# Kernel tuning notes

Hardware: AMD Instinct MI355X
Metric: run time of the kernel (lower is better)

The kernel has to match this reference:

```python
import itertools
import jax, jax.numpy as jnp
import numpy as np

NUM_MOLS = 1024
N_ATOMS = 32  # atoms per molecule (< 50 per module's precomputed edge_indices)
Z_DIM = 64
HIDDEN = 256
NUM_ATOM_TYPES = 10
NUM_BOND_TYPES = 5  # hparams['num_bond_types'] + 1
BN_EPS = 1e-5


def _build_edge_index():
    base = np.array(list(itertools.combinations(range(N_ATOMS), 2)), dtype=np.int64)  # [496, 2]
    offsets = (N_ATOMS * np.arange(NUM_MOLS, dtype=np.int64))[:, None, None]
    return jnp.asarray((base[None] + offsets).reshape(-1, 2))  # [E, 2]


def setup_inputs() -> dict:
    key = jax.random.key(0)
    ks = jax.random.split(key, 4)
    total_atoms = NUM_MOLS * N_ATOMS
    return {
        "z": jax.random.normal(ks[0], (total_atoms, Z_DIM), dtype=jnp.float32),
        "W1": jax.random.normal(ks[1], (Z_DIM, HIDDEN), dtype=jnp.float32) * 0.05,
        "b1": jnp.zeros((HIDDEN,), jnp.float32),
        "bn_gamma": jnp.ones((HIDDEN,), jnp.float32),
        "bn_beta": jnp.zeros((HIDDEN,), jnp.float32),
        "W2": jax.random.normal(ks[2], (HIDDEN, NUM_ATOM_TYPES), dtype=jnp.float32) * 0.05,
        "b2": jnp.zeros((NUM_ATOM_TYPES,), jnp.float32),
        "bond_matrix": jax.random.normal(ks[3], (NUM_BOND_TYPES, Z_DIM, Z_DIM), dtype=jnp.float32),
        "edge_index": _build_edge_index(),
    }


def reference(z, W1, b1, bn_gamma, bn_beta, W2, b2, bond_matrix, edge_index):
    # atom classifier: Linear -> BatchNorm1d (training-mode batch stats) -> GELU -> Linear
    h = z @ W1 + b1  # [A, H]
    mean = jnp.mean(h, axis=0)
    var = jnp.mean((h - mean) ** 2, axis=0)  # biased variance, as torch BN
    h = (h - mean) * jax.lax.rsqrt(var + BN_EPS) * bn_gamma + bn_beta
    h = jax.nn.gelu(h, approximate=False)
    atom_types = h @ W2 + b2  # [A, num_atom_types]

    # symmetric bond matrices, per-edge bilinear quadratic form, softmax over bond types
    W = 0.5 * (bond_matrix + jnp.swapaxes(bond_matrix, 1, 2))  # [T, d, d]
    z1 = z[edge_index[:, 0]]  # [E, d]
    z2 = z[edge_index[:, 1]]  # [E, d]
    logits = jnp.einsum('ed,tdc,ec->et', z1, W, z2)  # [E, T]
    edge_types = jax.nn.softmax(logits, axis=1)
    return atom_types, edge_types
```

## Files before the change

kernel.cpp:

```cpp
#include <hip/hip_runtime.h>
#include <hip/hip_bf16.h>
#include <math.h>

#define NM 1024
#define NA 32
#define ZD 64
#define HD 256
#define AT 10
#define BT 5
#define NROWS (NM*NA)
#define EPM 496
#define ATOM_OUT (NROWS*AT)


__global__ __launch_bounds__(256) void k1_moments(const float* __restrict__ z,
                                                  float* __restrict__ Msum,
                                                  float* __restrict__ sumz) {
    __shared__ __align__(16) float zs[128][64];
    __shared__ float sred[4][64];
    const int tid = threadIdx.x;
    const int d0 = (tid >> 4) << 2;
    const int e0 = (tid & 15) << 2;
    const int d = tid & 63, rq = tid >> 6;
    float acc[4][4] = {};
    float colsum = 0.f;
    for (int chunk = 0; chunk < 2; ++chunk) {
        const int rowbase = (blockIdx.x * 2 + chunk) * 128;
        __syncthreads();
        const float4* zg4 = (const float4*)(z + rowbase * 64);
        float4* zs4 = (float4*)zs;
        #pragma unroll
        for (int k = 0; k < 8; ++k) zs4[tid + (k << 8)] = zg4[tid + (k << 8)];
        __syncthreads();
        for (int r = 0; r < 128; ++r) {
            float4 a4 = *(const float4*)&zs[r][d0];
            float4 b4 = *(const float4*)&zs[r][e0];
            float a[4] = {a4.x, a4.y, a4.z, a4.w};
            float b[4] = {b4.x, b4.y, b4.z, b4.w};
            #pragma unroll
            for (int i = 0; i < 4; ++i)
                #pragma unroll
                for (int jj = 0; jj < 4; ++jj) acc[i][jj] += a[i] * b[jj];
        }
        for (int r = rq * 32; r < rq * 32 + 32; ++r) colsum += zs[r][d];
    }
    #pragma unroll
    for (int i = 0; i < 4; ++i)
        #pragma unroll
        for (int jj = 0; jj < 4; ++jj)
            atomicAdd(&Msum[(d0 + i) * 64 + (e0 + jj)], acc[i][jj]);
    sred[rq][d] = colsum;
    __syncthreads();
    if (tid < 64)
        atomicAdd(&sumz[tid], sred[0][tid] + sred[1][tid] + sred[2][tid] + sred[3][tid]);
}

__global__ __launch_bounds__(256) void k2w(const float* __restrict__ Msum,
                                           const float* __restrict__ sumz,
                                           const float* __restrict__ W1,
                                           const float* __restrict__ gamma,
                                           const float* __restrict__ beta,
                                           const float* __restrict__ bond,
                                           float* __restrict__ avec,
                                           float* __restrict__ cvec,
                                           float* __restrict__ Wsym) {
    const int tid = threadIdx.x;
    if (blockIdx.x >= 64) {
        int idx = ((int)blockIdx.x - 64) * 256 + tid;
        int t = idx >> 12, rem = idx & 4095, dd = rem >> 6, c = rem & 63;
        Wsym[idx] = 0.5f * (bond[(t << 12) + (dd << 6) + c] +
                            bond[(t << 12) + (c << 6) + dd]);
        return;
    }
    const int wv = tid >> 6, d = tid & 63;
    const int j = blockIdx.x * 4 + wv;
    const float wdj = W1[d * HD + j];
    float v = 0.f;
    for (int e = 0; e < 64; ++e) v += Msum[d * 64 + e] * W1[e * HD + j];
    float q = v * wdj;
    float s = sumz[d] * wdj;
    #pragma unroll
    for (int off = 32; off >= 1; off >>= 1) {
        q += __shfl_down(q, off);
        s += __shfl_down(s, off);
    }
    if (d == 0) {
        const float invN = 1.f / (float)NROWS;
        float mean = s * invN;
        float var = q * invN - mean * mean;
        float a = gamma[j] * rsqrtf(var + 1e-5f);
        avec[j] = a;
        cvec[j] = beta[j] - mean * a;
    }
}

__global__ __launch_bounds__(256) void k3_mlp(const float* __restrict__ z,
                                              const float* __restrict__ W1,
                                              const float* __restrict__ W2,
                                              const float* __restrict__ b2,
                                              const float* __restrict__ avec,
                                              const float* __restrict__ cvec,
                                              float* __restrict__ out_atom) {
    __shared__ __align__(16) float zsT[64][36];
    __shared__ __align__(16) float w1s[16][256];
    __shared__ float w2s[256][11];
    __shared__ float as[256], cs[256];
    const int tid = threadIdx.x;
    const int rowbase = blockIdx.x * 32;
    {
        const float* zp = z + (size_t)(rowbase + (tid >> 3)) * 64 + (tid & 7) * 8;
        float4 v0 = *(const float4*)zp;
        float4 v1 = *(const float4*)(zp + 4);
        const int r = tid >> 3, dbase = (tid & 7) * 8;
        zsT[dbase + 0][r] = v0.x; zsT[dbase + 1][r] = v0.y;
        zsT[dbase + 2][r] = v0.z; zsT[dbase + 3][r] = v0.w;
        zsT[dbase + 4][r] = v1.x; zsT[dbase + 5][r] = v1.y;
        zsT[dbase + 6][r] = v1.z; zsT[dbase + 7][r] = v1.w;
    }
    for (int k = tid; k < HD * AT; k += 256) w2s[k / 10][k % 10] = W2[k];
    as[tid] = avec[tid]; cs[tid] = cvec[tid];

    const int rg = tid >> 4, cg = tid & 15;
    const int r0 = rg << 1;
    float acc[2][4][4] = {};
    for (int ch = 0; ch < 4; ++ch) {
        __syncthreads();
        #pragma unroll
        for (int k = 0; k < 16; ++k) {
            int idx = tid + (k << 8);
            ((float*)w1s)[idx] = W1[(ch << 12) + idx];
        }
        __syncthreads();
        #pragma unroll
        for (int dl = 0; dl < 16; ++dl) {
            float zr0 = zsT[(ch << 4) + dl][r0];
            float zr1 = zsT[(ch << 4) + dl][r0 + 1];
            #pragma unroll
            for (int cb = 0; cb < 4; ++cb) {
                float4 wv = *(const float4*)&w1s[dl][(cb << 6) + (cg << 2)];
                float wr[4] = {wv.x, wv.y, wv.z, wv.w};
                #pragma unroll
                for (int u = 0; u < 4; ++u) {
                    acc[0][cb][u] += zr0 * wr[u];
                    acc[1][cb][u] += zr1 * wr[u];
                }
            }
        }
    }
    float p[2][10] = {};
    #pragma unroll
    for (int cb = 0; cb < 4; ++cb)
        #pragma unroll
        for (int u = 0; u < 4; ++u) {
            const int c = (cb << 6) + (cg << 2) + u;
            const float a = as[c], cc = cs[c];
            #pragma unroll
            for (int ri = 0; ri < 2; ++ri) {
                float h = acc[ri][cb][u] * a + cc;
                h = 0.5f * h * (1.0f + erff(h * 0.70710678118654752f));
                #pragma unroll
                for (int o = 0; o < 10; ++o) p[ri][o] += h * w2s[c][o];
            }
        }
    #pragma unroll
    for (int m = 1; m <= 8; m <<= 1)
        #pragma unroll
        for (int ri = 0; ri < 2; ++ri)
            #pragma unroll
            for (int o = 0; o < 10; ++o) p[ri][o] += __shfl_xor(p[ri][o], m);
    if (cg == 0) {
        #pragma unroll
        for (int ri = 0; ri < 2; ++ri)
            for (int o = 0; o < 10; ++o)
                out_atom[(size_t)(rowbase + r0 + ri) * AT + o] = p[ri][o] + b2[o];
    }
}

__global__ __launch_bounds__(512) void k4_edges(const float* __restrict__ z,
                                                const float* __restrict__ Wsym,
                                                float* __restrict__ out_edge) {
    __shared__ float zs[2][32][66];
    __shared__ float uT[2][5][32][18];
    const int tid = threadIdx.x;
    const int mol0 = blockIdx.x * 2;
    {
        const float2* zg2 = (const float2*)(z + (size_t)mol0 * 2048);
        #pragma unroll
        for (int k = 0; k < 4; ++k) {
            int e = tid + (k << 9);
            int ml = e >> 10, r = (e >> 5) & 31, c2 = e & 31;
            float2 v = zg2[e];
            zs[ml][r][c2 * 2] = v.x;
            zs[ml][r][c2 * 2 + 1] = v.y;
        }
    }
    const int wv = __builtin_amdgcn_readfirstlane(tid >> 6);
    const int lane = tid & 63;
    const int molA = lane >> 5, jA = lane & 31;
    const int mlB = tid >> 8;
    const int jg = tid & 31;
    const int i0 = ((tid >> 5) & 7) << 2;
    float accE[5][4] = {};
    __syncthreads();

    for (int qd = 0; qd < 4; ++qd) {
        float accA[5][2] = {};
        const int dpos = (qd << 4) + (wv << 1);
        for (int cb = 0; cb < 4; ++cb) {
            float zr[16];
            #pragma unroll
            for (int m = 0; m < 8; ++m) {
                float2 v = *(const float2*)&zs[molA][jA][(cb << 4) + (m << 1)];
                zr[m * 2] = v.x; zr[m * 2 + 1] = v.y;
            }
            #pragma unroll
            for (int t = 0; t < 5; ++t) {
                const float* wbase = Wsym + (size_t)(t << 12) + (size_t)(cb << 10) + dpos;
                #pragma unroll
                for (int cc = 0; cc < 16; ++cc) {
                    float w0 = wbase[cc * 64];
                    float w1 = wbase[cc * 64 + 1];
                    accA[t][0] += w0 * zr[cc];
                    accA[t][1] += w1 * zr[cc];
                }
            }
        }
        __syncthreads();
        #pragma unroll
        for (int t = 0; t < 5; ++t) {
            float2 w; w.x = accA[t][0]; w.y = accA[t][1];
            *(float2*)&uT[molA][t][jA][wv << 1] = w;
        }
        __syncthreads();
        #pragma unroll
        for (int cq = 0; cq < 4; ++cq) {
            const int gd = (qd << 4) + (cq << 2);
            float zc[4][4];
            #pragma unroll
            for (int ri = 0; ri < 4; ++ri) {
                float2 a = *(const float2*)&zs[mlB][i0 + ri][gd];
                float2 b = *(const float2*)&zs[mlB][i0 + ri][gd + 2];
                zc[ri][0] = a.x; zc[ri][1] = a.y; zc[ri][2] = b.x; zc[ri][3] = b.y;
            }
            #pragma unroll
            for (int t = 0; t < 5; ++t) {
                float2 ua = *(const float2*)&uT[mlB][t][jg][cq << 2];
                float2 ub = *(const float2*)&uT[mlB][t][jg][(cq << 2) + 2];
                #pragma unroll
                for (int ri = 0; ri < 4; ++ri)
                    accE[t][ri] += zc[ri][0] * ua.x + zc[ri][1] * ua.y
                                 + zc[ri][2] * ub.x + zc[ri][3] * ub.y;
            }
        }
    }
    const int ebase = (mol0 + mlB) * EPM;
    #pragma unroll
    for (int ri = 0; ri < 4; ++ri) {
        const int i = i0 + ri, j = jg;
        if (i < j) {
            float l0 = accE[0][ri], l1 = accE[1][ri], l2 = accE[2][ri];
            float l3 = accE[3][ri], l4 = accE[4][ri];
            float m = fmaxf(fmaxf(fmaxf(l0, l1), fmaxf(l2, l3)), l4);
            float e0 = expf(l0 - m), e1 = expf(l1 - m), e2 = expf(l2 - m);
            float e3 = expf(l3 - m), e4 = expf(l4 - m);
            float inv = 1.0f / (e0 + e1 + e2 + e3 + e4);
            int p = 31 * i - ((i * (i - 1)) >> 1) + (j - i - 1);
            float* o = out_edge + (size_t)(ebase + p) * 5;
            o[0] = e0 * inv; o[1] = e1 * inv; o[2] = e2 * inv;
            o[3] = e3 * inv; o[4] = e4 * inv;
        }
    }
}

extern "C" void kernel_launch(void* const* d_in, const int* in_sizes, int n_in,
                              void* d_out, int out_size, void* d_ws, size_t ws_size,
                              hipStream_t stream) {
    (void)in_sizes; (void)n_in; (void)out_size; (void)ws_size;
    const float* z     = (const float*)d_in[0];
    const float* W1    = (const float*)d_in[1];
    const float* gamma = (const float*)d_in[3];
    const float* beta  = (const float*)d_in[4];
    const float* W2    = (const float*)d_in[5];
    const float* b2    = (const float*)d_in[6];
    const float* bond  = (const float*)d_in[7];
    float* out = (float*)d_out;
    float* ws  = (float*)d_ws;

    float* Msum = ws;
    float* sumz = ws + 4096;
    float* avec = ws + 4160;
    float* cvec = ws + 4416;
    float* Wsym = ws + 4672;

    hipMemsetAsync(ws, 0, (4096 + 64) * sizeof(float), stream);
    k1_moments<<<128, 256, 0, stream>>>(z, Msum, sumz);
    k2w<<<144, 256, 0, stream>>>(Msum, sumz, W1, gamma, beta, bond, avec, cvec, Wsym);
    k3_mlp<<<1024, 256, 0, stream>>>(z, W1, W2, b2, avec, cvec, out);
    k4_edges<<<512, 512, 0, stream>>>(z, Wsym, out + ATOM_OUT);
}
```

Before: 240.1 us.

## Stage symmetric bond matrices in swizzled LDS and retile edge kernel

The edge kernel now loads each 64x64 bond matrix into shared memory with an XOR swizzle instead of reading it from global memory inside the inner loop. It computes U = z·W per bond type with 4x4 register tiles, then the per-pair quadratic forms with float4 LDS reads. The block drops from 512 to 256 threads and each thread accumulates 4x2 pairs, loop order changes from d-quarters to bond types. The aim is to cut repeated global/L2 weight traffic and raise arithmetic intensity, at the cost of more LDS per block (about 50KB) and more syncthreads.

```diff
diff --git a/kernel.cpp b/kernel.cpp
--- a/kernel.cpp
+++ b/kernel.cpp
@@ -176,98 +176,98 @@
     }
 }
 
-__global__ __launch_bounds__(512) void k4_edges(const float* __restrict__ z,
+__global__ __launch_bounds__(256) void k4_edges(const float* __restrict__ z,
                                                 const float* __restrict__ Wsym,
                                                 float* __restrict__ out_edge) {
-    __shared__ float zs[2][32][66];
-    __shared__ float uT[2][5][32][18];
+    __shared__ __align__(16) float zs[2][32][68];
+    __shared__ __align__(16) float WsL[4096];
+    __shared__ __align__(16) float Us[2][32][68];
     const int tid = threadIdx.x;
     const int mol0 = blockIdx.x * 2;
     {
-        const float2* zg2 = (const float2*)(z + (size_t)mol0 * 2048);
+        const float4* zg4 = (const float4*)(z + (size_t)mol0 * 2048);
         #pragma unroll
         for (int k = 0; k < 4; ++k) {
-            int e = tid + (k << 9);
-            int ml = e >> 10, r = (e >> 5) & 31, c2 = e & 31;
-            float2 v = zg2[e];
-            zs[ml][r][c2 * 2] = v.x;
-            zs[ml][r][c2 * 2 + 1] = v.y;
-        }
-    }
-    const int wv = __builtin_amdgcn_readfirstlane(tid >> 6);
-    const int lane = tid & 63;
-    const int molA = lane >> 5, jA = lane & 31;
-    const int mlB = tid >> 8;
-    const int jg = tid & 31;
-    const int i0 = ((tid >> 5) & 7) << 2;
-    float accE[5][4] = {};
-    __syncthreads();
-
-    for (int qd = 0; qd < 4; ++qd) {
-        float accA[5][2] = {};
-        const int dpos = (qd << 4) + (wv << 1);
-        for (int cb = 0; cb < 4; ++cb) {
-            float zr[16];
-            #pragma unroll
-            for (int m = 0; m < 8; ++m) {
-                float2 v = *(const float2*)&zs[molA][jA][(cb << 4) + (m << 1)];
-                zr[m * 2] = v.x; zr[m * 2 + 1] = v.y;
-            }
-            #pragma unroll
-            for (int t = 0; t < 5; ++t) {
-                const float* wbase = Wsym + (size_t)(t << 12) + (size_t)(cb << 10) + dpos;
-                #pragma unroll
-                for (int cc = 0; cc < 16; ++cc) {
-                    float w0 = wbase[cc * 64];
-                    float w1 = wbase[cc * 64 + 1];
-                    accA[t][0] += w0 * zr[cc];
-                    accA[t][1] += w1 * zr[cc];
+            int e = tid + (k << 8);
+            int ml = e >> 9, r = (e >> 4) & 31, c4 = e & 15;
+            *(float4*)&zs[ml][r][c4 << 2] = zg4[e];
+        }
+    }
+    const int am  = tid >> 7;
+    const int aj0 = ((tid >> 4) & 7) << 2;
+    const int adg = tid & 15;
+    const int ad0 = adg << 2;
+    const int bm  = tid >> 7;
+    const int i0  = ((tid >> 4) & 7) << 2;
+    const int j1  = tid & 15, j2 = j1 + 16;
+    float accE[5][4][2] = {};
+
+    const float4* wg4 = (const float4*)Wsym;
+    #pragma unroll
+    for (int t = 0; t < 5; ++t) {
+        #pragma unroll
+        for (int k = 0; k < 4; ++k) {
+            int e = tid + (k << 8);
+            int r = e >> 4, cq = e & 15;
+            *(float4*)&WsL[(r << 6) + ((cq ^ (r >> 2)) << 2)] = wg4[(t << 10) + e];
+        }
+        __syncthreads();
+        {
+            float acc[4][4] = {};
+            #pragma unroll
+            for (int cq = 0; cq < 16; ++cq) {
+                float4 zv[4];
+                #pragma unroll
+                for (int jj = 0; jj < 4; ++jj)
+                    zv[jj] = *(const float4*)&zs[am][aj0 + jj][cq << 2];
+                const int swz = (cq ^ adg) << 2;
+                #pragma unroll
+                for (int dd = 0; dd < 4; ++dd) {
+                    float4 wv = *(const float4*)&WsL[((ad0 + dd) << 6) + swz];
+                    #pragma unroll
+                    for (int jj = 0; jj < 4; ++jj)
+                        acc[jj][dd] += zv[jj].x * wv.x + zv[jj].y * wv.y
+                                     + zv[jj].z * wv.z + zv[jj].w * wv.w;
                 }
             }
-        }
-        __syncthreads();
-        #pragma unroll
-        for (int t = 0; t < 5; ++t) {
-            float2 w; w.x = accA[t][0]; w.y = accA[t][1];
-            *(float2*)&uT[molA][t][jA][wv << 1] = w;
-        }
-        __syncthreads();
-        #pragma unroll
-        for (int cq = 0; cq < 4; ++cq) {
-            const int gd = (qd << 4) + (cq << 2);
-            float zc[4][4];
+            #pragma unroll
+            for (int jj = 0; jj < 4; ++jj) {
+                float4 o; o.x = acc[jj][0]; o.y = acc[jj][1];
+                o.z = acc[jj][2]; o.w = acc[jj][3];
+                *(float4*)&Us[am][aj0 + jj][ad0] = o;
+            }
+        }
+        __syncthreads();
+        #pragma unroll
+        for (int dq = 0; dq < 16; ++dq) {
+            float4 u1 = *(const float4*)&Us[bm][j1][dq << 2];
+            float4 u2 = *(const float4*)&Us[bm][j2][dq << 2];
             #pragma unroll
             for (int ri = 0; ri < 4; ++ri) {
-                float2 a = *(const float2*)&zs[mlB][i0 + ri][gd];
-                float2 b = *(const float2*)&zs[mlB][i0 + ri][gd + 2];
-                zc[ri][0] = a.x; zc[ri][1] = a.y; zc[ri][2] = b.x; zc[ri][3] = b.y;
-            }
-            #pragma unroll
-            for (int t = 0; t < 5; ++t) {
-                float2 ua = *(const float2*)&uT[mlB][t][jg][cq << 2];
-                float2 ub = *(const float2*)&uT[mlB][t][jg][(cq << 2) + 2];
-                #pragma unroll
-                for (int ri = 0; ri < 4; ++ri)
-                    accE[t][ri] += zc[ri][0] * ua.x + zc[ri][1] * ua.y
-                                 + zc[ri][2] * ub.x + zc[ri][3] * ub.y;
-            }
-        }
-    }
-    const int ebase = (mol0 + mlB) * EPM;
+                float4 zv = *(const float4*)&zs[bm][i0 + ri][dq << 2];
+                accE[t][ri][0] += zv.x * u1.x + zv.y * u1.y + zv.z * u1.z + zv.w * u1.w;
+                accE[t][ri][1] += zv.x * u2.x + zv.y * u2.y + zv.z * u2.z + zv.w * u2.w;
+            }
+        }
+        __syncthreads();
+    }
     #pragma unroll
     for (int ri = 0; ri < 4; ++ri) {
-        const int i = i0 + ri, j = jg;
-        if (i < j) {
-            float l0 = accE[0][ri], l1 = accE[1][ri], l2 = accE[2][ri];
-            float l3 = accE[3][ri], l4 = accE[4][ri];
-            float m = fmaxf(fmaxf(fmaxf(l0, l1), fmaxf(l2, l3)), l4);
-            float e0 = expf(l0 - m), e1 = expf(l1 - m), e2 = expf(l2 - m);
-            float e3 = expf(l3 - m), e4 = expf(l4 - m);
-            float inv = 1.0f / (e0 + e1 + e2 + e3 + e4);
-            int p = 31 * i - ((i * (i - 1)) >> 1) + (j - i - 1);
-            float* o = out_edge + (size_t)(ebase + p) * 5;
-            o[0] = e0 * inv; o[1] = e1 * inv; o[2] = e2 * inv;
-            o[3] = e3 * inv; o[4] = e4 * inv;
+        #pragma unroll
+        for (int rj = 0; rj < 2; ++rj) {
+            const int i = i0 + ri, j = (rj == 0) ? j1 : j2;
+            if (i < j) {
+                float l0 = accE[0][ri][rj], l1 = accE[1][ri][rj], l2 = accE[2][ri][rj];
+                float l3 = accE[3][ri][rj], l4 = accE[4][ri][rj];
+                float m = fmaxf(fmaxf(fmaxf(l0, l1), fmaxf(l2, l3)), l4);
+                float e0 = expf(l0 - m), e1 = expf(l1 - m), e2 = expf(l2 - m);
+                float e3 = expf(l3 - m), e4 = expf(l4 - m);
+                float inv = 1.0f / (e0 + e1 + e2 + e3 + e4);
+                int p = 31 * i - ((i * (i - 1)) >> 1) + (j - i - 1);
+                float* o = out_edge + (size_t)((mol0 + bm) * EPM + p) * 5;
+                o[0] = e0 * inv; o[1] = e1 * inv; o[2] = e2 * inv;
+                o[3] = e3 * inv; o[4] = e4 * inv;
+            }
         }
     }
 }
@@ -296,5 +296,5 @@
     k1_moments<<<128, 256, 0, stream>>>(z, Msum, sumz);
     k2w<<<144, 256, 0, stream>>>(Msum, sumz, W1, gamma, beta, bond, avec, cvec, Wsym);
     k3_mlp<<<1024, 256, 0, stream>>>(z, W1, W2, b2, avec, cvec, out);
-    k4_edges<<<512, 512, 0, stream>>>(z, Wsym, out + ATOM_OUT);
-}
+    k4_edges<<<512, 256, 0, stream>>>(z, Wsym, out + ATOM_OUT);
+}
```

New measurement: 806.3 us. 3.36x slower.
